# Performance work log

Hardware: AMD Instinct MI355X
Metric: run time of the kernel (lower is better)

The kernel has to match this reference:

```python
import jax, jax.numpy as jnp
import numpy as np


def setup_inputs() -> dict:
    key = jax.random.key(0)
    k1, k2 = jax.random.split(key)
    x = jax.random.normal(k1, (16, 4096, 3), dtype=jnp.float32)  # [B, N, 3]
    y = jax.random.normal(k2, (16, 4096, 3), dtype=jnp.float32)  # [B, M, 3]
    return {"x": x, "y": y}


def reference(x, y):
    # Squared pairwise distances via the ||x||^2 + ||y||^2 - 2<x,y> expansion.
    # d: [B, N, M]
    x2 = jnp.sum(x * x, axis=-1)  # [B, N]
    y2 = jnp.sum(y * y, axis=-1)  # [B, M]
    xy = jnp.einsum('bnd,bmd->bnm', x, y)  # [B, N, M]
    d = x2[:, :, None] + y2[:, None, :] - 2.0 * xy
    # directed Chamfer terms: mean over own points of min sq-dist to other cloud
    dist_to_y = jnp.mean(jnp.min(d, axis=2), axis=1)  # [B] (x -> y)
    dist_to_x = jnp.mean(jnp.min(d, axis=1), axis=1)  # [B] (y -> x)
    # per-cloud max of the two directed distances, averaged over batch
    return jnp.mean(jnp.maximum(dist_to_y, dist_to_x))
```

## Files before the change

kernel.cpp:

```cpp
#include <hip/hip_runtime.h>


typedef __attribute__((ext_vector_type(8)))  short bf16x8;
typedef __attribute__((ext_vector_type(4)))  float f32x4;
typedef __attribute__((ext_vector_type(16))) float f32x16;

#define BATCH   16
#define NPTS    4096
#define DB      (2 * BATCH)
#define AF_U4   (DB * 128 * 64)
#define GM_F32  (2 * DB * NPTS)

static __device__ __forceinline__ unsigned bf16rn(float f) {
  unsigned u = __float_as_uint(f);
  return (u + 0x7FFFu + ((u >> 16) & 1u)) >> 16;
}
static __device__ __forceinline__ float bf2f(unsigned h) {
  return __uint_as_float(h << 16);
}
static __device__ __forceinline__ unsigned pk(unsigned lo, unsigned hi) {
  return (lo & 0xFFFFu) | (hi << 16);
}

__global__ __launch_bounds__(256) void chamfer_prep(
    const float* __restrict__ x, const float* __restrict__ y,
    uint4* __restrict__ af, unsigned* __restrict__ cnt) {
  const int idx = blockIdx.x * 256 + threadIdx.x;
  if (idx == 0) *cnt = 0;
  const int db = idx >> 12, m = idx & (NPTS - 1);
  const int dir = db >> 4, b = db & 15;
  const float* other = (dir == 0 ? y : x) + (size_t)b * NPTS * 3;
  float y0 = other[m * 3 + 0], y1 = other[m * 3 + 1], y2 = other[m * 3 + 2];
  float wv = fmaf(y2, y2, fmaf(y1, y1, y0 * y0));
  float z0 = -2.f * y0, z1 = -2.f * y1, z2 = -2.f * y2;
  unsigned h0 = bf16rn(z0), h1 = bf16rn(z1), h2 = bf16rn(z2);
  unsigned e0 = bf16rn(z0 - bf2f(h0));
  unsigned e1 = bf16rn(z1 - bf2f(h1));
  unsigned e2 = bf16rn(z2 - bf2f(h2));
  unsigned wh = bf16rn(wv), wl = bf16rn(wv - bf2f(wh));
  const int tile = m >> 5, row = m & 31;
  const size_t t0 = (size_t)(db * 128 + tile) * 64 + row;
  af[t0]      = make_uint4(pk(h0, h1), pk(h2, e0), pk(e1, e2), pk(h0, h1));
  af[t0 + 32] = make_uint4(pk(h2, wh), pk(wl, 0u), 0u, 0u);
}

__global__ __launch_bounds__(512, 4) void chamfer_mm(
    const float* __restrict__ x, const float* __restrict__ y,
    const uint4* __restrict__ af, float* __restrict__ gm) {
  const int bid = blockIdx.x;
  const int db  = bid >> 4;
  const int r   = bid & 15;
  const int c   = r >> 1;
  const int h   = r & 1;
  const int dir = db >> 4, b = db & 15;
  const float* own = (dir == 0 ? x : y) + (size_t)b * NPTS * 3;

  const int tid = threadIdx.x, w = tid >> 6, l = tid & 63;
  const int col = l & 31, kh = l >> 5;
  const unsigned ONE = 0x3F80u;

  bf16x8 bfr[2];
  float sq[2], rmn[2];
  #pragma unroll
  for (int nt = 0; nt < 2; ++nt) {
    const int n = c * 512 + w * 64 + nt * 32 + col;
    float a0 = own[n * 3 + 0], a1 = own[n * 3 + 1], a2 = own[n * 3 + 2];
    sq[nt]  = fmaf(a2, a2, fmaf(a1, a1, a0 * a0));
    rmn[nt] = 1e30f;
    unsigned h0 = bf16rn(a0), h1 = bf16rn(a1), h2 = bf16rn(a2);
    unsigned e0 = bf16rn(a0 - bf2f(h0));
    unsigned e1 = bf16rn(a1 - bf2f(h1));
    unsigned e2 = bf16rn(a2 - bf2f(h2));
    union { unsigned uu[4]; bf16x8 v; } U;
    U.uu[0] = (kh == 0) ? pk(h0, h1) : pk(e2, ONE);
    U.uu[1] = (kh == 0) ? pk(h2, h0) : pk(ONE, 0u);
    U.uu[2] = (kh == 0) ? pk(h1, h2) : 0u;
    U.uu[3] = (kh == 0) ? pk(e0, e1) : 0u;
    bfr[nt] = U.v;
  }

  const uint4* qa = af + ((size_t)(db * 128 + h * 64) * 64 + l);
  const f32x16 z16 = {0.f, 0.f, 0.f, 0.f, 0.f, 0.f, 0.f, 0.f,
                      0.f, 0.f, 0.f, 0.f, 0.f, 0.f, 0.f, 0.f};

  #pragma unroll 2
  for (int mt = 0; mt < 64; ++mt) {
    union { uint4 u; bf16x8 v; } A;
    A.u = qa[(size_t)mt * 64];
    #pragma unroll
    for (int nt = 0; nt < 2; ++nt) {
      f32x16 acc = __builtin_amdgcn_mfma_f32_32x32x16_bf16(
          A.v, bfr[nt], z16, 0, 0, 0);
      float m0 = fminf(fminf(acc[0],  acc[1]),  acc[2]);
      float m1 = fminf(fminf(acc[3],  acc[4]),  acc[5]);
      float m2 = fminf(fminf(acc[6],  acc[7]),  acc[8]);
      float m3 = fminf(fminf(acc[9],  acc[10]), acc[11]);
      float m4 = fminf(fminf(acc[12], acc[13]), acc[14]);
      float m5 = fminf(fminf(acc[15], m0), m1);
      float m6 = fminf(fminf(m2, m3), m4);
      rmn[nt] = fminf(fminf(m5, m6), rmn[nt]);
    }
  }

  #pragma unroll
  for (int nt = 0; nt < 2; ++nt) {
    float v = fminf(rmn[nt], __shfl_xor(rmn[nt], 32, 64));
    float sv = v + sq[nt];
    if (l < 32)
      gm[(size_t)(h * DB + db) * NPTS + c * 512 + w * 64 + nt * 32 + col] = sv;
  }
}

__global__ __launch_bounds__(256) void chamfer_combine(
    const float* __restrict__ gm, float* __restrict__ dist,
    unsigned* __restrict__ cnt, float* __restrict__ out) {
  const int db = blockIdx.x;
  const float* g0 = gm + (size_t)db * NPTS;
  const float* g1 = gm + (size_t)(DB + db) * NPTS;
  float s = 0.0f;
  for (int i = threadIdx.x; i < NPTS; i += 256)
    s += fminf(g0[i], g1[i]);
  #pragma unroll
  for (int off = 32; off > 0; off >>= 1) s += __shfl_down(s, off, 64);
  __shared__ float red[4];
  const int lane = threadIdx.x & 63, wid = threadIdx.x >> 6;
  if (lane == 0) red[wid] = s;
  __syncthreads();
  if (threadIdx.x == 0) {
    dist[db] = ((red[0] + red[1]) + (red[2] + red[3])) * (1.0f / (float)NPTS);
    __threadfence();
    unsigned old = __hip_atomic_fetch_add(cnt, 1u, __ATOMIC_ACQ_REL,
                                          __HIP_MEMORY_SCOPE_AGENT);
    if (old == DB - 1) {
      __threadfence();
      float acc = 0.0f;
      #pragma unroll
      for (int b = 0; b < BATCH; ++b) {
        float d0 = __uint_as_float(__hip_atomic_load(
            (const unsigned*)&dist[b], __ATOMIC_RELAXED,
            __HIP_MEMORY_SCOPE_AGENT));
        float d1 = __uint_as_float(__hip_atomic_load(
            (const unsigned*)&dist[b + BATCH], __ATOMIC_RELAXED,
            __HIP_MEMORY_SCOPE_AGENT));
        acc += fmaxf(d0, d1);
      }
      out[0] = acc * (1.0f / (float)BATCH);
    }
  }
}

#define TPB10    512
#define NT10     4
#define NPW10    (NT10 * 16)
#define NPB10    (8 * NPW10)
#define NBLK10   (DB * (NPTS / NPB10))
#define MCHUNK10 1024
#define MTILES10 (MCHUNK10 / 16)
#define LDSB10   (16 + MTILES10 * 512)

__global__ __launch_bounds__(TPB10) void chamfer_mfma10(
    const float* __restrict__ x, const float* __restrict__ y,
    float* __restrict__ gm) {
  __shared__ __align__(16) unsigned char lds[LDSB10];
  const int bid = blockIdx.x;
  const int db  = bid >> 3;
  const int nb  = bid & 7;
  const int dir = db >> 4;
  const int b   = db & 15;
  const float* own   = (dir == 0 ? x : y) + (size_t)b * NPTS * 3;
  const float* other = (dir == 0 ? y : x) + (size_t)b * NPTS * 3;
  const int tid = threadIdx.x, w = tid >> 6, l = tid & 63;
  const int col = l & 15, g = l >> 4;
  if (tid < 4) *(unsigned*)&lds[tid * 4] = 0u;
  bf16x8 bfrag[NT10];
  float  sq[NT10], rmn[NT10];
  #pragma unroll
  for (int nt = 0; nt < NT10; ++nt) {
    const int n = nb * NPB10 + w * NPW10 + nt * 16 + col;
    float a0 = own[n * 3 + 0], a1 = own[n * 3 + 1], a2 = own[n * 3 + 2];
    sq[nt]  = fmaf(a2, a2, fmaf(a1, a1, a0 * a0));
    rmn[nt] = 1e30f;
    unsigned h0 = bf16rn(a0), h1 = bf16rn(a1), h2 = bf16rn(a2);
    unsigned e0 = bf16rn(a0 - bf2f(h0));
    unsigned e1 = bf16rn(a1 - bf2f(h1));
    unsigned e2 = bf16rn(a2 - bf2f(h2));
    const unsigned ONE = 0x3F80u;
    unsigned u0, u1, u2, u3;
    if (g == 0)      { u0 = pk(h0, h1); u1 = pk(h2, h0);
                       u2 = pk(h1, h2); u3 = pk(e0, e1); }
    else if (g == 1) { u0 = pk(e2, ONE); u1 = pk(ONE, 0u); u2 = 0u; u3 = 0u; }
    else             { u0 = u1 = u2 = u3 = 0u; }
    union { unsigned uu[4]; bf16x8 v; } U;
    U.uu[0] = u0; U.uu[1] = u1; U.uu[2] = u2; U.uu[3] = u3;
    bfrag[nt] = U.v;
  }
  const int abase = (l < 32) ? (16 + l * 16) : 0;
  const int astep = (l < 32) ? 512 : 0;
  for (int mc = 0; mc < NPTS / MCHUNK10; ++mc) {
    __syncthreads();
    #pragma unroll
    for (int k2 = 0; k2 < 2; ++k2) {
      const int p  = tid * 2 + k2;
      const int pg = mc * MCHUNK10 + p;
      float y0 = other[pg * 3 + 0], y1 = other[pg * 3 + 1],
            y2 = other[pg * 3 + 2];
      float wv = fmaf(y2, y2, fmaf(y1, y1, y0 * y0));
      float z0 = -2.f * y0, z1 = -2.f * y1, z2 = -2.f * y2;
      unsigned h0 = bf16rn(z0), h1 = bf16rn(z1), h2 = bf16rn(z2);
      unsigned e0 = bf16rn(z0 - bf2f(h0));
      unsigned e1 = bf16rn(z1 - bf2f(h1));
      unsigned e2 = bf16rn(z2 - bf2f(h2));
      unsigned wh = bf16rn(wv), wl = bf16rn(wv - bf2f(wh));
      const int t = p >> 4, c = p & 15;
      *(uint4*)&lds[16 + t * 512 + c * 16] =
          make_uint4(pk(h0, h1), pk(h2, e0), pk(e1, e2), pk(h0, h1));
      *(uint4*)&lds[16 + t * 512 + (c + 16) * 16] =
          make_uint4(pk(h2, wh), pk(wl, 0u), 0u, 0u);
    }
    __syncthreads();
    #pragma unroll 2
    for (int t = 0; t < MTILES10; ++t) {
      const bf16x8 afv = *(const bf16x8*)&lds[abase + t * astep];
      #pragma unroll
      for (int nt = 0; nt < NT10; ++nt) {
        f32x4 z = {0.f, 0.f, 0.f, 0.f};
        f32x4 acc = __builtin_amdgcn_mfma_f32_16x16x32_bf16(
            afv, bfrag[nt], z, 0, 0, 0);
        float mloc = fminf(fminf(acc[0], acc[1]), acc[2]);
        rmn[nt] = fminf(fminf(rmn[nt], acc[3]), mloc);
      }
    }
  }
  float s = 0.f;
  #pragma unroll
  for (int nt = 0; nt < NT10; ++nt) {
    float v = rmn[nt];
    v = fminf(v, __shfl_xor(v, 16, 64));
    v = fminf(v, __shfl_xor(v, 32, 64));
    s += v + sq[nt];
  }
  #pragma unroll
  for (int m = 1; m <= 8; m <<= 1) s += __shfl_xor(s, m, 64);
  if (l == 0) gm[db * 64 + nb * 8 + w] = s;
}

__global__ __launch_bounds__(1024) void chamfer_fin10(
    const float* __restrict__ gm, float* __restrict__ out) {
  __shared__ float dls[DB];
  const int t = threadIdx.x;
  const int db = t >> 5, j = t & 31;
  float v = gm[db * 64 + j] + gm[db * 64 + j + 32];
  #pragma unroll
  for (int m = 1; m <= 16; m <<= 1) v += __shfl_xor(v, m, 64);
  if (j == 0) dls[db] = v * (1.0f / (float)NPTS);
  __syncthreads();
  if (t < BATCH) {
    float mx = fmaxf(dls[t], dls[t + BATCH]);
    #pragma unroll
    for (int m = 1; m <= 8; m <<= 1) mx += __shfl_xor(mx, m, 64);
    if (t == 0) out[0] = mx * (1.0f / (float)BATCH);
  }
}

extern "C" void kernel_launch(void* const* d_in, const int* in_sizes, int n_in,
                              void* d_out, int out_size, void* d_ws, size_t ws_size,
                              hipStream_t stream) {
  const float* x = (const float*)d_in[0];
  const float* y = (const float*)d_in[1];
  float* out = (float*)d_out;

  const size_t need = (size_t)AF_U4 * 16 + (size_t)GM_F32 * 4 + DB * 4 + 4;
  if (ws_size >= need) {
    uint4* af     = (uint4*)d_ws;
    float* gm     = (float*)((char*)d_ws + (size_t)AF_U4 * 16);
    float* dist   = gm + GM_F32;
    unsigned* cnt = (unsigned*)(dist + DB);
    chamfer_prep<<<512, 256, 0, stream>>>(x, y, af, cnt);
    chamfer_mm<<<512, 512, 0, stream>>>(x, y, af, gm);
    chamfer_combine<<<DB, 256, 0, stream>>>(gm, dist, cnt, out);
  } else {
    float* gm = (float*)d_ws;
    chamfer_mfma10<<<NBLK10, TPB10, 0, stream>>>(x, y, gm);
    chamfer_fin10<<<1, 1024, 0, stream>>>(gm, out);
  }
}
```

Baseline: 36.86 us.

## Fuse prep pass into matmul kernel, staging other-cloud fragments in LDS

The separate prep kernel that encoded the other point cloud into split-bf16 fragments in global memory is removed. Each matmul block now encodes its own half of the other cloud (2048 points) directly into a 64KB shared-memory buffer and reads its A fragments from LDS. This removes one kernel launch and a global write/read round trip. The cost is redundant encoding across the 8 blocks sharing a half, plus larger LDS use that may limit occupancy. The unused fallback path is deleted and the loop unroll is raised to 4.

```diff
diff --git a/kernel.cpp b/kernel.cpp
--- a/kernel.cpp
+++ b/kernel.cpp
@@ -2,13 +2,11 @@
 
 
 typedef __attribute__((ext_vector_type(8)))  short bf16x8;
-typedef __attribute__((ext_vector_type(4)))  float f32x4;
 typedef __attribute__((ext_vector_type(16))) float f32x16;
 
 #define BATCH   16
 #define NPTS    4096
 #define DB      (2 * BATCH)
-#define AF_U4   (DB * 128 * 64)
 #define GM_F32  (2 * DB * NPTS)
 
 static __device__ __forceinline__ unsigned bf16rn(float f) {
@@ -22,43 +20,45 @@
   return (lo & 0xFFFFu) | (hi << 16);
 }
 
-__global__ __launch_bounds__(256) void chamfer_prep(
-    const float* __restrict__ x, const float* __restrict__ y,
-    uint4* __restrict__ af, unsigned* __restrict__ cnt) {
-  const int idx = blockIdx.x * 256 + threadIdx.x;
-  if (idx == 0) *cnt = 0;
-  const int db = idx >> 12, m = idx & (NPTS - 1);
-  const int dir = db >> 4, b = db & 15;
-  const float* other = (dir == 0 ? y : x) + (size_t)b * NPTS * 3;
-  float y0 = other[m * 3 + 0], y1 = other[m * 3 + 1], y2 = other[m * 3 + 2];
-  float wv = fmaf(y2, y2, fmaf(y1, y1, y0 * y0));
-  float z0 = -2.f * y0, z1 = -2.f * y1, z2 = -2.f * y2;
-  unsigned h0 = bf16rn(z0), h1 = bf16rn(z1), h2 = bf16rn(z2);
-  unsigned e0 = bf16rn(z0 - bf2f(h0));
-  unsigned e1 = bf16rn(z1 - bf2f(h1));
-  unsigned e2 = bf16rn(z2 - bf2f(h2));
-  unsigned wh = bf16rn(wv), wl = bf16rn(wv - bf2f(wh));
-  const int tile = m >> 5, row = m & 31;
-  const size_t t0 = (size_t)(db * 128 + tile) * 64 + row;
-  af[t0]      = make_uint4(pk(h0, h1), pk(h2, e0), pk(e1, e2), pk(h0, h1));
-  af[t0 + 32] = make_uint4(pk(h2, wh), pk(wl, 0u), 0u, 0u);
-}
-
 __global__ __launch_bounds__(512, 4) void chamfer_mm(
     const float* __restrict__ x, const float* __restrict__ y,
-    const uint4* __restrict__ af, float* __restrict__ gm) {
+    float* __restrict__ gm, unsigned* __restrict__ cnt) {
+  __shared__ __align__(16) uint4 afl[64 * 64];
+
   const int bid = blockIdx.x;
+  const int tid = threadIdx.x;
+  if (bid == 0 && tid == 0) *cnt = 0;
+
   const int db  = bid >> 4;
   const int r   = bid & 15;
   const int c   = r >> 1;
   const int h   = r & 1;
   const int dir = db >> 4, b = db & 15;
-  const float* own = (dir == 0 ? x : y) + (size_t)b * NPTS * 3;
+  const float* own   = (dir == 0 ? x : y) + (size_t)b * NPTS * 3;
+  const float* other = (dir == 0 ? y : x) + (size_t)b * NPTS * 3;
+  const float* mp    = other + (size_t)h * 2048 * 3;
 
-  const int tid = threadIdx.x, w = tid >> 6, l = tid & 63;
+  #pragma unroll
+  for (int k = 0; k < 4; ++k) {
+    const int p = tid + k * 512;
+    float y0 = mp[p * 3 + 0], y1 = mp[p * 3 + 1], y2 = mp[p * 3 + 2];
+    float wv = fmaf(y2, y2, fmaf(y1, y1, y0 * y0));
+    float z0 = -2.f * y0, z1 = -2.f * y1, z2 = -2.f * y2;
+    unsigned h0 = bf16rn(z0), h1 = bf16rn(z1), h2 = bf16rn(z2);
+    unsigned e0 = bf16rn(z0 - bf2f(h0));
+    unsigned e1 = bf16rn(z1 - bf2f(h1));
+    unsigned e2 = bf16rn(z2 - bf2f(h2));
+    unsigned wh = bf16rn(wv), wl = bf16rn(wv - bf2f(wh));
+    const int tile = p >> 5, row = p & 31;
+    afl[tile * 64 + row]      =
+        make_uint4(pk(h0, h1), pk(h2, e0), pk(e1, e2), pk(h0, h1));
+    afl[tile * 64 + 32 + row] =
+        make_uint4(pk(h2, wh), pk(wl, 0u), 0u, 0u);
+  }
+
+  const int w = tid >> 6, l = tid & 63;
   const int col = l & 31, kh = l >> 5;
   const unsigned ONE = 0x3F80u;
-
   bf16x8 bfr[2];
   float sq[2], rmn[2];
   #pragma unroll
@@ -78,15 +78,15 @@
     U.uu[3] = (kh == 0) ? pk(e0, e1) : 0u;
     bfr[nt] = U.v;
   }
+  __syncthreads();
 
-  const uint4* qa = af + ((size_t)(db * 128 + h * 64) * 64 + l);
+  const int aoff = kh * 32 + col;
   const f32x16 z16 = {0.f, 0.f, 0.f, 0.f, 0.f, 0.f, 0.f, 0.f,
                       0.f, 0.f, 0.f, 0.f, 0.f, 0.f, 0.f, 0.f};
-
-  #pragma unroll 2
+  #pragma unroll 4
   for (int mt = 0; mt < 64; ++mt) {
     union { uint4 u; bf16x8 v; } A;
-    A.u = qa[(size_t)mt * 64];
+    A.u = afl[mt * 64 + aoff];
     #pragma unroll
     for (int nt = 0; nt < 2; ++nt) {
       f32x16 acc = __builtin_amdgcn_mfma_f32_32x32x16_bf16(
@@ -149,119 +149,6 @@
   }
 }
 
-#define TPB10    512
-#define NT10     4
-#define NPW10    (NT10 * 16)
-#define NPB10    (8 * NPW10)
-#define NBLK10   (DB * (NPTS / NPB10))
-#define MCHUNK10 1024
-#define MTILES10 (MCHUNK10 / 16)
-#define LDSB10   (16 + MTILES10 * 512)
-
-__global__ __launch_bounds__(TPB10) void chamfer_mfma10(
-    const float* __restrict__ x, const float* __restrict__ y,
-    float* __restrict__ gm) {
-  __shared__ __align__(16) unsigned char lds[LDSB10];
-  const int bid = blockIdx.x;
-  const int db  = bid >> 3;
-  const int nb  = bid & 7;
-  const int dir = db >> 4;
-  const int b   = db & 15;
-  const float* own   = (dir == 0 ? x : y) + (size_t)b * NPTS * 3;
-  const float* other = (dir == 0 ? y : x) + (size_t)b * NPTS * 3;
-  const int tid = threadIdx.x, w = tid >> 6, l = tid & 63;
-  const int col = l & 15, g = l >> 4;
-  if (tid < 4) *(unsigned*)&lds[tid * 4] = 0u;
-  bf16x8 bfrag[NT10];
-  float  sq[NT10], rmn[NT10];
-  #pragma unroll
-  for (int nt = 0; nt < NT10; ++nt) {
-    const int n = nb * NPB10 + w * NPW10 + nt * 16 + col;
-    float a0 = own[n * 3 + 0], a1 = own[n * 3 + 1], a2 = own[n * 3 + 2];
-    sq[nt]  = fmaf(a2, a2, fmaf(a1, a1, a0 * a0));
-    rmn[nt] = 1e30f;
-    unsigned h0 = bf16rn(a0), h1 = bf16rn(a1), h2 = bf16rn(a2);
-    unsigned e0 = bf16rn(a0 - bf2f(h0));
-    unsigned e1 = bf16rn(a1 - bf2f(h1));
-    unsigned e2 = bf16rn(a2 - bf2f(h2));
-    const unsigned ONE = 0x3F80u;
-    unsigned u0, u1, u2, u3;
-    if (g == 0)      { u0 = pk(h0, h1); u1 = pk(h2, h0);
-                       u2 = pk(h1, h2); u3 = pk(e0, e1); }
-    else if (g == 1) { u0 = pk(e2, ONE); u1 = pk(ONE, 0u); u2 = 0u; u3 = 0u; }
-    else             { u0 = u1 = u2 = u3 = 0u; }
-    union { unsigned uu[4]; bf16x8 v; } U;
-    U.uu[0] = u0; U.uu[1] = u1; U.uu[2] = u2; U.uu[3] = u3;
-    bfrag[nt] = U.v;
-  }
-  const int abase = (l < 32) ? (16 + l * 16) : 0;
-  const int astep = (l < 32) ? 512 : 0;
-  for (int mc = 0; mc < NPTS / MCHUNK10; ++mc) {
-    __syncthreads();
-    #pragma unroll
-    for (int k2 = 0; k2 < 2; ++k2) {
-      const int p  = tid * 2 + k2;
-      const int pg = mc * MCHUNK10 + p;
-      float y0 = other[pg * 3 + 0], y1 = other[pg * 3 + 1],
-            y2 = other[pg * 3 + 2];
-      float wv = fmaf(y2, y2, fmaf(y1, y1, y0 * y0));
-      float z0 = -2.f * y0, z1 = -2.f * y1, z2 = -2.f * y2;
-      unsigned h0 = bf16rn(z0), h1 = bf16rn(z1), h2 = bf16rn(z2);
-      unsigned e0 = bf16rn(z0 - bf2f(h0));
-      unsigned e1 = bf16rn(z1 - bf2f(h1));
-      unsigned e2 = bf16rn(z2 - bf2f(h2));
-      unsigned wh = bf16rn(wv), wl = bf16rn(wv - bf2f(wh));
-      const int t = p >> 4, c = p & 15;
-      *(uint4*)&lds[16 + t * 512 + c * 16] =
-          make_uint4(pk(h0, h1), pk(h2, e0), pk(e1, e2), pk(h0, h1));
-      *(uint4*)&lds[16 + t * 512 + (c + 16) * 16] =
-          make_uint4(pk(h2, wh), pk(wl, 0u), 0u, 0u);
-    }
-    __syncthreads();
-    #pragma unroll 2
-    for (int t = 0; t < MTILES10; ++t) {
-      const bf16x8 afv = *(const bf16x8*)&lds[abase + t * astep];
-      #pragma unroll
-      for (int nt = 0; nt < NT10; ++nt) {
-        f32x4 z = {0.f, 0.f, 0.f, 0.f};
-        f32x4 acc = __builtin_amdgcn_mfma_f32_16x16x32_bf16(
-            afv, bfrag[nt], z, 0, 0, 0);
-        float mloc = fminf(fminf(acc[0], acc[1]), acc[2]);
-        rmn[nt] = fminf(fminf(rmn[nt], acc[3]), mloc);
-      }
-    }
-  }
-  float s = 0.f;
-  #pragma unroll
-  for (int nt = 0; nt < NT10; ++nt) {
-    float v = rmn[nt];
-    v = fminf(v, __shfl_xor(v, 16, 64));
-    v = fminf(v, __shfl_xor(v, 32, 64));
-    s += v + sq[nt];
-  }
-  #pragma unroll
-  for (int m = 1; m <= 8; m <<= 1) s += __shfl_xor(s, m, 64);
-  if (l == 0) gm[db * 64 + nb * 8 + w] = s;
-}
-
-__global__ __launch_bounds__(1024) void chamfer_fin10(
-    const float* __restrict__ gm, float* __restrict__ out) {
-  __shared__ float dls[DB];
-  const int t = threadIdx.x;
-  const int db = t >> 5, j = t & 31;
-  float v = gm[db * 64 + j] + gm[db * 64 + j + 32];
-  #pragma unroll
-  for (int m = 1; m <= 16; m <<= 1) v += __shfl_xor(v, m, 64);
-  if (j == 0) dls[db] = v * (1.0f / (float)NPTS);
-  __syncthreads();
-  if (t < BATCH) {
-    float mx = fmaxf(dls[t], dls[t + BATCH]);
-    #pragma unroll
-    for (int m = 1; m <= 8; m <<= 1) mx += __shfl_xor(mx, m, 64);
-    if (t == 0) out[0] = mx * (1.0f / (float)BATCH);
-  }
-}
-
 extern "C" void kernel_launch(void* const* d_in, const int* in_sizes, int n_in,
                               void* d_out, int out_size, void* d_ws, size_t ws_size,
                               hipStream_t stream) {
@@ -269,18 +156,10 @@
   const float* y = (const float*)d_in[1];
   float* out = (float*)d_out;
 
-  const size_t need = (size_t)AF_U4 * 16 + (size_t)GM_F32 * 4 + DB * 4 + 4;
-  if (ws_size >= need) {
-    uint4* af     = (uint4*)d_ws;
-    float* gm     = (float*)((char*)d_ws + (size_t)AF_U4 * 16);
-    float* dist   = gm + GM_F32;
-    unsigned* cnt = (unsigned*)(dist + DB);
-    chamfer_prep<<<512, 256, 0, stream>>>(x, y, af, cnt);
-    chamfer_mm<<<512, 512, 0, stream>>>(x, y, af, gm);
-    chamfer_combine<<<DB, 256, 0, stream>>>(gm, dist, cnt, out);
-  } else {
-    float* gm = (float*)d_ws;
-    chamfer_mfma10<<<NBLK10, TPB10, 0, stream>>>(x, y, gm);
-    chamfer_fin10<<<1, 1024, 0, stream>>>(gm, out);
-  }
+  float* gm     = (float*)d_ws;
+  float* dist   = gm + GM_F32;
+  unsigned* cnt = (unsigned*)(dist + DB);
+
+  chamfer_mm<<<512, 512, 0, stream>>>(x, y, gm, cnt);
+  chamfer_combine<<<DB, 256, 0, stream>>>(gm, dist, cnt, out);
 }
```

Result: faster. 29.81 us (-19.1%).
